# Kernel tuning notes

Measured on AMD Instinct MI355X. Metric: run time of the kernel, lower is better.

## Reference

```python
import jax, jax.numpy as jnp
import numpy as np

D = 8192          # Hadamard dimension (power of 2)
K = 1024          # number of selected columns = len(idx)
NORMALIZED = True
SCALE = np.float32(1.0 / np.sqrt(D))


def setup_inputs() -> dict:
    key = jax.random.key(0)
    k1, k2 = jax.random.split(key)
    u = jax.random.normal(k1, (4, 2048, K), dtype=jnp.float32)
    idx = jnp.sort(jax.random.randint(k2, (K,), 0, D, dtype=jnp.int32))
    return {"u": u, "idx": idx}


def _fwht(x):
    """Unnormalized fast Walsh-Hadamard transform over last dim. x: (B, D)."""
    B, d = x.shape
    h = 1
    while h < d:  # log2(D) static iterations -> jit-friendly
        y = x.reshape(B, d // (2 * h), 2, h)
        a, b = y[:, :, 0, :], y[:, :, 1, :]
        x = jnp.stack([a + b, a - b], axis=2).reshape(B, d)
        h *= 2
    return x


def reference(u, idx):
    # x = H_D[:, idx] @ u  (optionally / sqrt(D))
    # = FWHT(scatter(u at idx into zeros(D))) since H @ e_j = H[:, j]
    orig = u.shape[:-1]
    u2 = u.reshape(-1, u.shape[-1])                      # (B, K)
    z = jnp.zeros((u2.shape[0], D), u.dtype).at[:, idx].add(u2)  # (B, D)
    out = _fwht(z)
    if NORMALIZED:
        out = out * SCALE
    return out.reshape(*orig, D)
```

## Files before the change

### kernel.cpp

```cpp
#include <hip/hip_runtime.h>

#define D      8192
#define K      1024
#define BLOCK  256
#define GRID_MAX 2048
#define SCALE  0.011048543456039806f

typedef float nat_f4 __attribute__((ext_vector_type(4)));


__device__ __forceinline__ int swz4(int f) { return f ^ ((f >> 3) & 7); }

__device__ __forceinline__ void fwht32(float* x) {
#pragma unroll
    for (int s = 0; s < 5; ++s) {
        const int h = 1 << s;
#pragma unroll
        for (int g = 0; g < 32; g += 2 * h)
#pragma unroll
            for (int e = 0; e < h; ++e) {
                float a = x[g + e], b = x[g + e + h];
                x[g + e]     = a + b;
                x[g + e + h] = a - b;
            }
    }
}

__device__ __forceinline__ void fwht8(float* x) {
#pragma unroll
    for (int s = 0; s < 3; ++s) {
        const int h = 1 << s;
#pragma unroll
        for (int g = 0; g < 8; g += 2 * h)
#pragma unroll
            for (int e = 0; e < h; ++e) {
                float a = x[g + e], b = x[g + e + h];
                x[g + e]     = a + b;
                x[g + e + h] = a - b;
            }
    }
}

__global__ __launch_bounds__(BLOCK, 5)
void UpProjectFastHadamardTransform_80101140070867_kernel(
    const float* __restrict__ u, const int* __restrict__ idx,
    float* __restrict__ out, int nrows)
{
    __shared__ float4 lds4[D / 4];
    float* lds = (float*)lds4;
    const int T = threadIdx.x;
    const int w = T >> 6;
    const int l = T & 63;

    const int4 id = ((const int4*)idx)[T];

    const int ldsW   = w << 11;
    const int lds4W  = w << 9;
    const int c1     = T & 7;
    const int c2     = ((l << 1) + (l >> 5)) & 7;
    const int p1_lo2 = l >> 2, p1_hi = l >> 5, p1_e = l & 3;
    const int p2r_b4 = ((l & 31) << 4) + ((l >> 5) << 3);
    const int p2w_b  = ((((l >> 5) | (w << 1)) << 10) |
                        (((l >> 2) & 7) << 2) | (l & 3));

    int r = blockIdx.x;
    const int stride = (int)gridDim.x;
    float4 v = ((const float4*)(u + (size_t)r * K))[T];

    while (r < nrows) {
        __syncthreads();

#pragma unroll
        for (int q = 0; q < 8; ++q)
            lds4[(q << 8) + T] = make_float4(0.f, 0.f, 0.f, 0.f);
        __syncthreads();

        {
            int f, a;
            f = id.x >> 2; a = 4 * swz4(f) + (id.x & 3); atomicAdd(&lds[a], v.x);
            f = id.y >> 2; a = 4 * swz4(f) + (id.y & 3); atomicAdd(&lds[a], v.y);
            f = id.z >> 2; a = 4 * swz4(f) + (id.z & 3); atomicAdd(&lds[a], v.z);
            f = id.w >> 2; a = 4 * swz4(f) + (id.w & 3); atomicAdd(&lds[a], v.w);
        }

        const int rn = r + stride;
        if (rn < nrows) v = ((const float4*)(u + (size_t)rn * K))[T];
        __syncthreads();

        float x[32];

#pragma unroll
        for (int g = 0; g < 8; ++g) {
            const float4 a = lds4[(T << 3) + (g ^ c1)];
            x[4*g+0] = a.x; x[4*g+1] = a.y; x[4*g+2] = a.z; x[4*g+3] = a.w;
        }
        fwht32(x);
#pragma unroll
        for (int j = 0; j < 32; ++j) {
            const int f = (j << 4) + p1_lo2;
            lds[ldsW + 4 * (f ^ ((2 * j + p1_hi) & 7)) + p1_e] = x[j];
        }

#pragma unroll
        for (int g = 0; g < 8; ++g) {
            const float4 a = lds4[lds4W + p2r_b4 + (g ^ c2)];
            x[4*g+0] = a.x; x[4*g+1] = a.y; x[4*g+2] = a.z; x[4*g+3] = a.w;
        }
        fwht32(x);
#pragma unroll
        for (int m = 0; m < 32; ++m)
            lds[p2w_b + (m << 5)] = x[m];

        __syncthreads();

#pragma unroll
        for (int h = 0; h < 8; ++h) {
            const float4 a = lds4[(h << 8) + T];
            x[h] = a.x; x[8 + h] = a.y; x[16 + h] = a.z; x[24 + h] = a.w;
        }
#pragma unroll
        for (int q = 0; q < 4; ++q) fwht8(&x[q * 8]);

        float* orow = out + (size_t)r * D + ((T >> 3) * 32 + (T & 7) * 4);
#pragma unroll
        for (int e = 0; e < 8; ++e) {
            nat_f4 o = { x[e] * SCALE, x[8 + e] * SCALE,
                         x[16 + e] * SCALE, x[24 + e] * SCALE };
            __builtin_nontemporal_store(o, (nat_f4*)(orow + e * 1024));
        }

        r = rn;
    }
}

extern "C" void kernel_launch(void* const* d_in, const int* in_sizes, int n_in,
                              void* d_out, int out_size, void* d_ws, size_t ws_size,
                              hipStream_t stream) {
    const float* u   = (const float*)d_in[0];
    const int*   idx = (const int*)d_in[1];
    float*       out = (float*)d_out;
    const int rows = in_sizes[0] / K;
    const int grid = rows < GRID_MAX ? rows : GRID_MAX;
    hipLaunchKernelGGL(UpProjectFastHadamardTransform_80101140070867_kernel,
                       dim3(grid), dim3(BLOCK), 0, stream, u, idx, out, rows);
}
```

Baseline: 358.3 us.

## Make each wave own a 2048-slice, removing block barriers from the FWHT

The 8192-point transform is restructured so each of the four waves handles a 2048-element quarter on its own. Each wave scatters all 1024 inputs into its slice, folding the top two high-order Hadamard stages into sign flips precomputed per index. That removes every __syncthreads and the cross-wave third LDS pass. The last radix-2 stage becomes a DPP lane-exchange butterfly, and output becomes scalar non-temporal stores instead of float4. The cost is four times more LDS atomics per row, redundant global loads of u by each wave, and narrower, strided output stores.

```diff
diff --git a/kernel.cpp b/kernel.cpp
--- a/kernel.cpp
+++ b/kernel.cpp
@@ -6,10 +6,6 @@
 #define GRID_MAX 2048
 #define SCALE  0.011048543456039806f
 
-typedef float nat_f4 __attribute__((ext_vector_type(4)));
-
-
-__device__ __forceinline__ int swz4(int f) { return f ^ ((f >> 3) & 7); }
 
 __device__ __forceinline__ void fwht32(float* x) {
 #pragma unroll
@@ -26,19 +22,9 @@
     }
 }
 
-__device__ __forceinline__ void fwht8(float* x) {
-#pragma unroll
-    for (int s = 0; s < 3; ++s) {
-        const int h = 1 << s;
-#pragma unroll
-        for (int g = 0; g < 8; g += 2 * h)
-#pragma unroll
-            for (int e = 0; e < h; ++e) {
-                float a = x[g + e], b = x[g + e + h];
-                x[g + e]     = a + b;
-                x[g + e + h] = a - b;
-            }
-    }
+__device__ __forceinline__ float bfly_xor1(float x, float sgn) {
+    const int yi = __builtin_amdgcn_mov_dpp(__float_as_int(x), 0xB1, 0xF, 0xF, true);
+    return __builtin_fmaf(sgn, x, __int_as_float(yi));
 }
 
 __global__ __launch_bounds__(BLOCK, 5)
@@ -46,87 +32,93 @@
     const float* __restrict__ u, const int* __restrict__ idx,
     float* __restrict__ out, int nrows)
 {
-    __shared__ float4 lds4[D / 4];
-    float* lds = (float*)lds4;
+    __shared__ float lds[D];
     const int T = threadIdx.x;
     const int w = T >> 6;
     const int l = T & 63;
 
-    const int4 id = ((const int4*)idx)[T];
+    float*  q  = lds + (w << 11);
+    float4* q4 = (float4*)q;
 
-    const int ldsW   = w << 11;
-    const int lds4W  = w << 9;
-    const int c1     = T & 7;
-    const int c2     = ((l << 1) + (l >> 5)) & 7;
-    const int p1_lo2 = l >> 2, p1_hi = l >> 5, p1_e = l & 3;
-    const int p2r_b4 = ((l & 31) << 4) + ((l >> 5) << 3);
-    const int p2w_b  = ((((l >> 5) | (w << 1)) << 10) |
-                        (((l >> 2) & 7) << 2) | (l & 3));
+    int pk[16];
+    {
+        const int4* idx4 = (const int4*)idx;
+#pragma unroll
+        for (int j = 0; j < 4; ++j) {
+            const int4 id = idx4[(l << 2) + j];
+            auto PACK = [&](int i) {
+                const int p = i & 2047, f = p >> 2;
+                const int word = 4 * (f ^ ((f >> 3) & 7)) + (p & 3);
+                const int sb = (i >> 11) & w;
+                return word | (((sb ^ (sb >> 1)) & 1) << 31);
+            };
+            pk[4*j+0] = PACK(id.x); pk[4*j+1] = PACK(id.y);
+            pk[4*j+2] = PACK(id.z); pk[4*j+3] = PACK(id.w);
+        }
+    }
 
     int r = blockIdx.x;
     const int stride = (int)gridDim.x;
-    float4 v = ((const float4*)(u + (size_t)r * K))[T];
+
+    float4 uv[4];
+    {
+        const float4* u4 = (const float4*)(u + (size_t)r * K);
+#pragma unroll
+        for (int j = 0; j < 4; ++j) uv[j] = u4[(l << 2) + j];
+    }
+
+    const int   c1  = l & 7;
+    const float sgn = (l & 1) ? -1.f : 1.f;
 
     while (r < nrows) {
-        __syncthreads();
+#pragma unroll
+        for (int j = 0; j < 8; ++j)
+            q4[(j << 6) + l] = make_float4(0.f, 0.f, 0.f, 0.f);
 
 #pragma unroll
-        for (int q = 0; q < 8; ++q)
-            lds4[(q << 8) + T] = make_float4(0.f, 0.f, 0.f, 0.f);
-        __syncthreads();
-
-        {
-            int f, a;
-            f = id.x >> 2; a = 4 * swz4(f) + (id.x & 3); atomicAdd(&lds[a], v.x);
-            f = id.y >> 2; a = 4 * swz4(f) + (id.y & 3); atomicAdd(&lds[a], v.y);
-            f = id.z >> 2; a = 4 * swz4(f) + (id.z & 3); atomicAdd(&lds[a], v.z);
-            f = id.w >> 2; a = 4 * swz4(f) + (id.w & 3); atomicAdd(&lds[a], v.w);
+        for (int j = 0; j < 4; ++j) {
+            const int p0 = pk[4*j+0], p1 = pk[4*j+1],
+                      p2 = pk[4*j+2], p3 = pk[4*j+3];
+            atomicAdd(&q[p0 & 2047], __int_as_float(__float_as_int(uv[j].x) ^ (p0 & 0x80000000)));
+            atomicAdd(&q[p1 & 2047], __int_as_float(__float_as_int(uv[j].y) ^ (p1 & 0x80000000)));
+            atomicAdd(&q[p2 & 2047], __int_as_float(__float_as_int(uv[j].z) ^ (p2 & 0x80000000)));
+            atomicAdd(&q[p3 & 2047], __int_as_float(__float_as_int(uv[j].w) ^ (p3 & 0x80000000)));
         }
 
         const int rn = r + stride;
-        if (rn < nrows) v = ((const float4*)(u + (size_t)rn * K))[T];
-        __syncthreads();
+        if (rn < nrows) {
+            const float4* u4 = (const float4*)(u + (size_t)rn * K);
+#pragma unroll
+            for (int j = 0; j < 4; ++j) uv[j] = u4[(l << 2) + j];
+        }
 
         float x[32];
 
 #pragma unroll
         for (int g = 0; g < 8; ++g) {
-            const float4 a = lds4[(T << 3) + (g ^ c1)];
+            const float4 a = q4[(l << 3) + (g ^ c1)];
             x[4*g+0] = a.x; x[4*g+1] = a.y; x[4*g+2] = a.z; x[4*g+3] = a.w;
         }
         fwht32(x);
+
 #pragma unroll
         for (int j = 0; j < 32; ++j) {
-            const int f = (j << 4) + p1_lo2;
-            lds[ldsW + 4 * (f ^ ((2 * j + p1_hi) & 7)) + p1_e] = x[j];
+            const int f = (j << 4) + (l >> 2);
+            q[4 * (f ^ ((2 * j + (l >> 5)) & 7)) + (l & 3)] = x[j];
         }
 
 #pragma unroll
         for (int g = 0; g < 8; ++g) {
-            const float4 a = lds4[lds4W + p2r_b4 + (g ^ c2)];
+            const float4 a = q4[(l << 3) + (g ^ c1)];
             x[4*g+0] = a.x; x[4*g+1] = a.y; x[4*g+2] = a.z; x[4*g+3] = a.w;
         }
         fwht32(x);
+
+        float* orow = out + (size_t)r * D + (w << 11) + ((l & 1) << 10) + (l >> 1);
 #pragma unroll
-        for (int m = 0; m < 32; ++m)
-            lds[p2w_b + (m << 5)] = x[m];
-
-        __syncthreads();
-
-#pragma unroll
-        for (int h = 0; h < 8; ++h) {
-            const float4 a = lds4[(h << 8) + T];
-            x[h] = a.x; x[8 + h] = a.y; x[16 + h] = a.z; x[24 + h] = a.w;
-        }
-#pragma unroll
-        for (int q = 0; q < 4; ++q) fwht8(&x[q * 8]);
-
-        float* orow = out + (size_t)r * D + ((T >> 3) * 32 + (T & 7) * 4);
-#pragma unroll
-        for (int e = 0; e < 8; ++e) {
-            nat_f4 o = { x[e] * SCALE, x[8 + e] * SCALE,
-                         x[16 + e] * SCALE, x[24 + e] * SCALE };
-            __builtin_nontemporal_store(o, (nat_f4*)(orow + e * 1024));
+        for (int m = 0; m < 32; ++m) {
+            const float t = bfly_xor1(x[m], sgn);
+            __builtin_nontemporal_store(t * SCALE, orow + (m << 5));
         }
 
         r = rn;
```

New measurement: 429.5 us. 19.9% more time.
